# Kernel tuning notes

Measured on AMD Instinct MI355X. Metric: run time of the kernel, lower is better.

The kernel has to match this reference:

```python
import jax, jax.numpy as jnp
import numpy as np

H = 16      # q heads
G = 4       # groups (n_rep)
THETA = 10000.0


def _rope(x, cos, sin):
    # x pairs adjacent elements (torch complex view of reshape(..., -1, 2))
    x0 = x[..., ::2]
    x1 = x[..., 1::2]
    r0 = x0 * cos - x1 * sin
    r1 = x0 * sin + x1 * cos
    return jnp.stack([r0, r1], axis=-1).reshape(x.shape)


def setup_inputs() -> dict:
    key = jax.random.key(0)
    ks = jax.random.split(key, 5)
    B, S, D = 2, 2048, 1024
    return {
        "x": jax.random.normal(ks[0], (B, S, D), jnp.float32),
        "Wq": jax.random.normal(ks[1], (D, D), jnp.float32) * 0.02,
        "Wk": jax.random.normal(ks[2], (D, D // G), jnp.float32) * 0.02,
        "Wv": jax.random.normal(ks[3], (D, D // G), jnp.float32) * 0.02,
        "Wo": jax.random.normal(ks[4], (D, D), jnp.float32) * 0.02,
    }


def reference(x, Wq, Wk, Wv, Wo):
    B, S, D = x.shape
    hd = D // H                     # head dim = 64
    Hkv = H // G                    # kv heads = 4

    q = x @ Wq                      # (B,S,D)
    k = x @ Wk                      # (B,S,D/G)
    v = x @ Wv                      # (B,S,D/G)

    # repeat_kv: (B,S,Hkv,hd) -> (B,S,H,hd)
    k = jnp.repeat(k.reshape(B, S, Hkv, hd), G, axis=2)
    v = jnp.repeat(v.reshape(B, S, Hkv, hd), G, axis=2)

    # RoPE angles: freqs precomputed over hidden_dim (as in source)
    inv = 1.0 / (THETA ** (jnp.arange(0, D, 2, dtype=jnp.float32) / D))  # (D/2,)
    ang = jnp.arange(S, dtype=jnp.float32)[:, None] * inv[None, :]       # (S,D/2)
    q = _rope(q, jnp.cos(ang)[None], jnp.sin(ang)[None])                 # (B,S,D)
    angk = ang[:, : hd // 2]                                             # (S,hd/2)
    k = _rope(k, jnp.cos(angk)[None, :, None, :], jnp.sin(angk)[None, :, None, :])

    q = q.reshape(B, S, H, hd).transpose(0, 2, 1, 3)   # (B,H,S,hd)
    k = k.transpose(0, 2, 1, 3)
    v = v.transpose(0, 2, 1, 3)

    # NOTE: scale uses sqrt(hidden_dim), faithful to source
    scores = jnp.einsum('bhqd,bhkd->bhqk', q, k) / jnp.sqrt(jnp.float32(D))
    p = jax.nn.softmax(scores, axis=-1)
    o = jnp.einsum('bhqk,bhkd->bhqd', p, v)
    o = o.transpose(0, 2, 1, 3).reshape(B, S, D)
    return o @ Wo
```

## Files before the change

### kernel.cpp

```cpp
#include <hip/hip_runtime.h>
#include <math.h>

#define BATCH 2
#define SEQ   2048
#define DMODEL 1024
#define KDIM  1024
#define NH    16
#define HDIM  64
#define GRP   4
#define NKV   4

enum { M_PLAIN = 0, M_QKV = 1 };

#define LN_THETA 9.210340371976184f
#define QSCALE 0.04508422002778f

typedef short bf8_t __attribute__((ext_vector_type(8)));
typedef float f4_t __attribute__((ext_vector_type(4)));
typedef unsigned short us4_t __attribute__((ext_vector_type(4)));
typedef unsigned short us8_t __attribute__((ext_vector_type(8)));

#define QB_OFF 0
#define KB_OFF 4194304
#define VB_OFF (4194304 + 1048576)

__device__ __forceinline__ unsigned short f2bf(float f) {
  unsigned int u = __float_as_uint(f);
  u += 0x7fffu + ((u >> 16) & 1u);
  return (unsigned short)(u >> 16);
}

__device__ __forceinline__ float fexp2(float x) {
#if __has_builtin(__builtin_amdgcn_exp2f)
  return __builtin_amdgcn_exp2f(x);
#else
  return exp2f(x);
#endif
}

__device__ __forceinline__ void gload_lds16(const void* g, void* l) {
  typedef __attribute__((address_space(1))) unsigned int gu32;
  typedef __attribute__((address_space(3))) unsigned int lu32;
  __builtin_amdgcn_global_load_lds((const gu32*)g, (lu32*)l, 16, 0, 0);
}

__global__ __launch_bounds__(256) void convT_all(const float* __restrict__ W0,
                                                 const float* __restrict__ W1,
                                                 const float* __restrict__ W2,
                                                 const float* __restrict__ W3,
                                                 unsigned short* __restrict__ Wqkvt,
                                                 unsigned short* __restrict__ Wot) {
  const float* W; unsigned short* out; int N, rowoff;
  switch (blockIdx.z) {
    case 0: W = W0; out = Wqkvt; N = 1024; rowoff = 0;    break;
    case 1: W = W1; out = Wqkvt; N = 256;  rowoff = 1024; break;
    case 2: W = W2; out = Wqkvt; N = 256;  rowoff = 1280; break;
    default: W = W3; out = Wot;  N = 1024; rowoff = 0;    break;
  }
  const int n0 = blockIdx.x * 64;
  if (n0 >= N) return;
  __shared__ unsigned short T[64][72];
  const int t = threadIdx.x;
  const int k0 = blockIdx.y * 64;
  const int kr = t >> 4, n4 = (t & 15) * 4;
#pragma unroll
  for (int i = 0; i < 4; ++i) {
    const int k = kr + i * 16;
    float4 v = *(const float4*)&W[(size_t)(k0 + k) * N + n0 + n4];
    T[n4 + 0][k] = f2bf(v.x);
    T[n4 + 1][k] = f2bf(v.y);
    T[n4 + 2][k] = f2bf(v.z);
    T[n4 + 3][k] = f2bf(v.w);
  }
  __syncthreads();
#pragma unroll
  for (int i = 0; i < 2; ++i) {
    const int c = t + i * 256;
    const int n = c >> 3, kc = (c & 7) * 8;
    us8_t v = *(const us8_t*)&T[n][kc];
    *(us8_t*)&out[(size_t)(rowoff + n0 + n) * KDIM + k0 + kc] = v;
  }
}

template <int MODE>
__global__ __launch_bounds__(512, 2) void gemm_bf16(const void* __restrict__ A_,
                                                    const unsigned short* __restrict__ Bt,
                                                    void* __restrict__ Cdst_, int N) {
  __shared__ __align__(16) unsigned short As[4 * 4096];
  __shared__ __align__(16) unsigned short Bs[4 * 4096];

  const int tid = threadIdx.x;
  const int lane = tid & 63, quad = lane >> 4, l16 = lane & 15;
  const int w = tid >> 6, wm = w >> 1, wn = w & 1;
  const int row0 = blockIdx.x * 128, col0 = blockIdx.y * 128;

  const int m0 = tid >> 2;
  const int kc0 = (tid & 3) ^ ((m0 >> 1) & 3);
  const unsigned short* Ag0 = (const unsigned short*)A_ + (size_t)(row0 + m0) * KDIM + kc0 * 8;
  const float*          Xg0 = (const float*)A_ + (size_t)(row0 + m0) * KDIM + kc0 * 8;
  const unsigned short* Bg0 = Bt + (size_t)(col0 + m0) * KDIM + kc0 * 8;
  unsigned short* Al0 = &As[tid * 8];
  unsigned short* Bl0 = &Bs[tid * 8];

#define STAGE_GEMM(kk)                                                   \
  do {                                                                   \
    _Pragma("unroll") for (int kh = 0; kh < 4; ++kh) {                   \
      if constexpr (MODE == M_QKV) {                                     \
        float4 a0 = *(const float4*)(Xg0 + (kk) + kh * 32);              \
        float4 a1 = *(const float4*)(Xg0 + (kk) + kh * 32 + 4);          \
        us8_t o8 = {f2bf(a0.x), f2bf(a0.y), f2bf(a0.z), f2bf(a0.w),      \
                    f2bf(a1.x), f2bf(a1.y), f2bf(a1.z), f2bf(a1.w)};     \
        *(us8_t*)(Al0 + kh * 4096) = o8;                                 \
      } else {                                                           \
        gload_lds16(Ag0 + (kk) + kh * 32, Al0 + kh * 4096);              \
      }                                                                  \
      gload_lds16(Bg0 + (kk) + kh * 32, Bl0 + kh * 4096);                \
    }                                                                    \
  } while (0)

  int aoff[2][4], boff[4][4];
#pragma unroll
  for (int mi = 0; mi < 2; ++mi) {
    const int am = wm * 32 + mi * 16 + l16;
    const int sw = quad ^ ((am >> 1) & 3);
#pragma unroll
    for (int kh = 0; kh < 4; ++kh)
      aoff[mi][kh] = kh * 4096 + (((am << 2) | sw) << 3);
  }
#pragma unroll
  for (int ni = 0; ni < 4; ++ni) {
    const int bn = wn * 64 + ni * 16 + l16;
    const int sw = quad ^ ((bn >> 1) & 3);
#pragma unroll
    for (int kh = 0; kh < 4; ++kh)
      boff[ni][kh] = kh * 4096 + (((bn << 2) | sw) << 3);
  }

  f4_t acc[2][4];
#pragma unroll
  for (int mi = 0; mi < 2; ++mi)
#pragma unroll
    for (int ni = 0; ni < 4; ++ni) acc[mi][ni] = (f4_t){0.f, 0.f, 0.f, 0.f};

  for (int kb = 0; kb < KDIM; kb += 128) {
    __syncthreads();
    STAGE_GEMM(kb);
    __syncthreads();

#pragma unroll
    for (int kh = 0; kh < 4; ++kh) {
      bf8_t af[2], bfr[4];
#pragma unroll
      for (int mi = 0; mi < 2; ++mi) af[mi] = *(const bf8_t*)&As[aoff[mi][kh]];
#pragma unroll
      for (int ni = 0; ni < 4; ++ni) bfr[ni] = *(const bf8_t*)&Bs[boff[ni][kh]];
#pragma unroll
      for (int mi = 0; mi < 2; ++mi)
#pragma unroll
        for (int ni = 0; ni < 4; ++ni)
          acc[mi][ni] = __builtin_amdgcn_mfma_f32_16x16x32_bf16(af[mi], bfr[ni], acc[mi][ni], 0, 0, 0);
    }
  }
#undef STAGE_GEMM

  if constexpr (MODE == M_PLAIN) {
    float* out = (float*)Cdst_;
#pragma unroll
    for (int mi = 0; mi < 2; ++mi) {
      const int rowb = row0 + wm * 32 + mi * 16 + quad * 4;
#pragma unroll
      for (int ni = 0; ni < 4; ++ni) {
        const int n = col0 + wn * 64 + ni * 16 + l16;
#pragma unroll
        for (int r = 0; r < 4; ++r)
          out[(size_t)(rowb + r) * N + n] = acc[mi][ni][r];
      }
    }
  } else {
    unsigned short* Qb = (unsigned short*)Cdst_;
    unsigned short* Kb = Qb + (KB_OFF - QB_OFF);
    unsigned short* Vb = Qb + (VB_OFF - QB_OFF);
#pragma unroll
    for (int ni = 0; ni < 4; ++ni) {
      const int nb = col0 + wn * 64 + ni * 16;
      const int n = nb + l16;
      if (nb < 1024) {
        const float inv = expf(-(float)(2 * (n >> 1)) * (LN_THETA / (float)DMODEL));
        const float sgn = (n & 1) ? 1.f : -1.f;
        const int h = n >> 6, d = n & 63;
#pragma unroll
        for (int mi = 0; mi < 2; ++mi) {
          const int rowb = row0 + wm * 32 + mi * 16 + quad * 4;
#pragma unroll
          for (int r = 0; r < 4; ++r) {
            const int row = rowb + r;
            const int bb = row >> 11, s = row & (SEQ - 1);
            const float v = acc[mi][ni][r];
            const float p = __shfl_xor(v, 1);
            float sn, cs;
            sincosf((float)s * inv, &sn, &cs);
            const float res = (v * cs + sgn * p * sn) * QSCALE;
            Qb[((size_t)(bb * NH + h) * SEQ + s) * HDIM + d] = f2bf(res);
          }
        }
      } else if (nb < 1280) {
        const int nk = n - 1024;
        const int hkv = nk >> 6, d = nk & 63;
        const float inv = expf(-(float)(2 * (d >> 1)) * (LN_THETA / (float)DMODEL));
        const float sgn = (nk & 1) ? 1.f : -1.f;
#pragma unroll
        for (int mi = 0; mi < 2; ++mi) {
          const int rowb = row0 + wm * 32 + mi * 16 + quad * 4;
#pragma unroll
          for (int r = 0; r < 4; ++r) {
            const int row = rowb + r;
            const int bb = row >> 11, s = row & (SEQ - 1);
            const float v = acc[mi][ni][r];
            const float p = __shfl_xor(v, 1);
            float sn, cs;
            sincosf((float)s * inv, &sn, &cs);
            const float res = v * cs + sgn * p * sn;
            Kb[((size_t)(bb * NKV + hkv) * SEQ + s) * HDIM + d] = f2bf(res);
          }
        }
      } else {
        const int nv = n - 1280;
        const int hkv = nv >> 6, d = nv & 63;
#pragma unroll
        for (int mi = 0; mi < 2; ++mi) {
          const int s0 = row0 + wm * 32 + mi * 16 + quad * 4;
          const int bb = s0 >> 11, sl = s0 & (SEQ - 1);
          const int st = sl & 63;
          const int ps = (sl & ~63) | (st & 0x20) | ((st & 0x0C) << 1) | ((st & 0x10) >> 2);
          us4_t stv = {f2bf(acc[mi][ni][0]), f2bf(acc[mi][ni][1]),
                       f2bf(acc[mi][ni][2]), f2bf(acc[mi][ni][3])};
          *(us4_t*)&Vb[((size_t)(bb * NKV + hkv) * HDIM + d) * SEQ + ps] = stv;
        }
      }
    }
  }
}

__global__ __launch_bounds__(256, 4) void attn_fwd(const unsigned short* __restrict__ Q,
                                                   const unsigned short* __restrict__ K,
                                                   const unsigned short* __restrict__ V,
                                                   unsigned short* __restrict__ Ow) {
  __shared__ __align__(16) unsigned short Kt[2 * 4096];
  __shared__ __align__(16) unsigned short Vt[2 * 4096];

  const int b = blockIdx.x >> 4;
  const int h = blockIdx.x & (NH - 1);
  const int hkv = h >> 2;
  const int q0 = blockIdx.y * 128;
  const int tid = threadIdx.x;
  const int w = tid >> 6;
  const int lane = tid & 63;
  const int quad = lane >> 4;
  const int l16 = lane & 15;

  const unsigned short* Qg = Q + ((size_t)(b * NH + h) * SEQ + q0 + w * 32) * HDIM;
  const unsigned short* Kg = K + (size_t)(b * NKV + hkv) * SEQ * HDIM;
  const unsigned short* Vg = V + (size_t)(b * NKV + hkv) * HDIM * SEQ;

  bf8_t qb[2][2];
#pragma unroll
  for (int g = 0; g < 2; ++g)
#pragma unroll
    for (int half = 0; half < 2; ++half)
      qb[g][half] = *(const bf8_t*)(Qg + (size_t)(g * 16 + l16) * HDIM + half * 32 + quad * 8);

  f4_t accO[2][4];
#pragma unroll
  for (int g = 0; g < 2; ++g)
#pragma unroll
    for (int d = 0; d < 4; ++d) accO[g][d] = (f4_t){0.f, 0.f, 0.f, 0.f};
  float accLs[2] = {0.f, 0.f};

  const int sw8 = (quad ^ ((l16 >> 1) & 3)) << 3;

  const int skey = tid >> 2;
  const int gc = ((tid & 3) ^ ((tid >> 3) & 3)) << 3;
  const unsigned short* KgA = Kg + (size_t)skey * HDIM + gc;
  const unsigned short* VgA = Vg + (size_t)skey * SEQ + gc;

#define STAGE_ATTN(c, kk)                                                          \
  do {                                                                             \
    gload_lds16(KgA + (size_t)(kk) * HDIM,      &Kt[(c) * 4096 + tid * 8]);        \
    gload_lds16(KgA + (size_t)(kk) * HDIM + 32, &Kt[(c) * 4096 + tid * 8 + 2048]); \
    gload_lds16(VgA + (kk),      &Vt[(c) * 4096 + tid * 8]);                       \
    gload_lds16(VgA + (kk) + 32, &Vt[(c) * 4096 + tid * 8 + 2048]);                \
  } while (0)

  STAGE_ATTN(0, 0);
  __syncthreads();
  int cur = 0;
  for (int k0 = 0; k0 < SEQ; k0 += 64) {
    if (k0 + 64 < SEQ) STAGE_ATTN(cur ^ 1, k0 + 64);

    const unsigned short* Ktc = Kt + cur * 4096;
    const unsigned short* Vtc = Vt + cur * 4096;

    union { bf8_t bf; unsigned int dw[4]; } pa[2][2];
#pragma unroll
    for (int cb = 0; cb < 4; ++cb) {
      const int koff = (cb * 16 + l16) * 32 + sw8;
      bf8_t kf0 = *(const bf8_t*)&Ktc[koff];
      bf8_t kf1 = *(const bf8_t*)&Ktc[koff + 2048];
#pragma unroll
      for (int g = 0; g < 2; ++g) {
        f4_t s = (f4_t){0.f, 0.f, 0.f, 0.f};
        s = __builtin_amdgcn_mfma_f32_16x16x32_bf16(kf0, qb[g][0], s, 0, 0, 0);
        s = __builtin_amdgcn_mfma_f32_16x16x32_bf16(kf1, qb[g][1], s, 0, 0, 0);
        const float p0 = fexp2(s[0]), p1 = fexp2(s[1]);
        const float p2 = fexp2(s[2]), p3 = fexp2(s[3]);
        accLs[g] += (p0 + p1) + (p2 + p3);
        unsigned int w0, w1;
        asm("v_cvt_pk_bf16_f32 %0, %1, %2" : "=v"(w0) : "v"(p0), "v"(p1));
        asm("v_cvt_pk_bf16_f32 %0, %1, %2" : "=v"(w1) : "v"(p2), "v"(p3));
        pa[g][cb >> 1].dw[(cb & 1) * 2 + 0] = w0;
        pa[g][cb >> 1].dw[(cb & 1) * 2 + 1] = w1;
      }
    }

#pragma unroll
    for (int db = 0; db < 4; ++db) {
      const int voff = (db * 16 + l16) * 32 + sw8;
      bf8_t vf0 = *(const bf8_t*)&Vtc[voff];
      bf8_t vf1 = *(const bf8_t*)&Vtc[voff + 2048];
#pragma unroll
      for (int g = 0; g < 2; ++g) {
        accO[g][db] = __builtin_amdgcn_mfma_f32_16x16x32_bf16(pa[g][0].bf, vf0, accO[g][db], 0, 0, 0);
        accO[g][db] = __builtin_amdgcn_mfma_f32_16x16x32_bf16(pa[g][1].bf, vf1, accO[g][db], 0, 0, 0);
      }
    }

    __syncthreads();
    cur ^= 1;
  }
#undef STAGE_ATTN

#pragma unroll
  for (int g = 0; g < 2; ++g) {
    accLs[g] += __shfl_xor(accLs[g], 16);
    accLs[g] += __shfl_xor(accLs[g], 32);
  }
  const float il0 = 1.0f / accLs[0];
  const float il1 = 1.0f / accLs[1];

#pragma unroll
  for (int g = 0; g < 2; ++g)
#pragma unroll
    for (int r = 0; r < 4; ++r) {
      const float ilr = __shfl(g ? il1 : il0, quad * 4 + r);
      const int q = q0 + w * 32 + g * 16 + quad * 4 + r;
      unsigned short* op = Ow + (((size_t)b * SEQ + q) * NH + h) * HDIM;
#pragma unroll
      for (int db = 0; db < 4; ++db)
        op[db * 16 + l16] = f2bf(accO[g][db][r] * ilr);
    }
}

extern "C" void kernel_launch(void* const* d_in, const int* in_sizes, int n_in,
                              void* d_out, int out_size, void* d_ws, size_t ws_size,
                              hipStream_t stream) {
  (void)in_sizes; (void)n_in; (void)out_size; (void)ws_size;
  const float* x  = (const float*)d_in[0];
  const float* Wq = (const float*)d_in[1];
  const float* Wk = (const float*)d_in[2];
  const float* Wv = (const float*)d_in[3];
  const float* Wo = (const float*)d_in[4];
  float* out = (float*)d_out;

  unsigned short* Qb    = (unsigned short*)d_ws;
  unsigned short* Kb    = Qb + 4194304;
  unsigned short* Vb    = Kb + 1048576;
  unsigned short* Owb   = Vb + 1048576;
  unsigned short* Wqkvt = Owb + 4194304;
  unsigned short* Wot   = Wqkvt + 1572864;

  dim3 blk(256);
  convT_all<<<dim3(16, 16, 4), blk, 0, stream>>>(Wq, Wk, Wv, Wo, Wqkvt, Wot);

  gemm_bf16<M_QKV><<<dim3(32, 12), dim3(512), 0, stream>>>(x, Wqkvt, Qb, 1536);
  attn_fwd<<<dim3(BATCH * NH, SEQ / 128), blk, 0, stream>>>(Qb, Kb, Vb, Owb);
  gemm_bf16<M_PLAIN><<<dim3(32, 8), dim3(512), 0, stream>>>(Owb, Wot, out, DMODEL);
}
```

Baseline: 163.8 us.

## Double-buffer GEMM LDS staging, pre-convert x to bf16, prioritize attention MFMAs

```diff
diff --git a/kernel.cpp b/kernel.cpp
--- a/kernel.cpp
+++ b/kernel.cpp
@@ -42,6 +42,14 @@
   typedef __attribute__((address_space(1))) unsigned int gu32;
   typedef __attribute__((address_space(3))) unsigned int lu32;
   __builtin_amdgcn_global_load_lds((const gu32*)g, (lu32*)l, 16, 0, 0);
+}
+
+__global__ __launch_bounds__(256) void conv_x(const float* __restrict__ in,
+                                              unsigned short* __restrict__ out) {
+  const int i = blockIdx.x * 256 + threadIdx.x;
+  float4 v = ((const float4*)in)[i];
+  us4_t o = {f2bf(v.x), f2bf(v.y), f2bf(v.z), f2bf(v.w)};
+  ((us4_t*)out)[i] = o;
 }
 
 __global__ __launch_bounds__(256) void convT_all(const float* __restrict__ W0,
@@ -83,11 +91,11 @@
 }
 
 template <int MODE>
-__global__ __launch_bounds__(512, 2) void gemm_bf16(const void* __restrict__ A_,
+__global__ __launch_bounds__(512, 2) void gemm_bf16(const unsigned short* __restrict__ A,
                                                     const unsigned short* __restrict__ Bt,
                                                     void* __restrict__ Cdst_, int N) {
-  __shared__ __align__(16) unsigned short As[4 * 4096];
-  __shared__ __align__(16) unsigned short Bs[4 * 4096];
+  __shared__ __align__(16) unsigned short As[2 * 8192];
+  __shared__ __align__(16) unsigned short Bs[2 * 8192];
 
   const int tid = threadIdx.x;
   const int lane = tid & 63, quad = lane >> 4, l16 = lane & 15;
@@ -96,35 +104,26 @@
 
   const int m0 = tid >> 2;
   const int kc0 = (tid & 3) ^ ((m0 >> 1) & 3);
-  const unsigned short* Ag0 = (const unsigned short*)A_ + (size_t)(row0 + m0) * KDIM + kc0 * 8;
-  const float*          Xg0 = (const float*)A_ + (size_t)(row0 + m0) * KDIM + kc0 * 8;
+  const unsigned short* Ag0 = A + (size_t)(row0 + m0) * KDIM + kc0 * 8;
   const unsigned short* Bg0 = Bt + (size_t)(col0 + m0) * KDIM + kc0 * 8;
   unsigned short* Al0 = &As[tid * 8];
   unsigned short* Bl0 = &Bs[tid * 8];
 
-#define STAGE_GEMM(kk)                                                   \
-  do {                                                                   \
-    _Pragma("unroll") for (int kh = 0; kh < 4; ++kh) {                   \
-      if constexpr (MODE == M_QKV) {                                     \
-        float4 a0 = *(const float4*)(Xg0 + (kk) + kh * 32);              \
-        float4 a1 = *(const float4*)(Xg0 + (kk) + kh * 32 + 4);          \
-        us8_t o8 = {f2bf(a0.x), f2bf(a0.y), f2bf(a0.z), f2bf(a0.w),      \
-                    f2bf(a1.x), f2bf(a1.y), f2bf(a1.z), f2bf(a1.w)};     \
-        *(us8_t*)(Al0 + kh * 4096) = o8;                                 \
-      } else {                                                           \
-        gload_lds16(Ag0 + (kk) + kh * 32, Al0 + kh * 4096);              \
-      }                                                                  \
-      gload_lds16(Bg0 + (kk) + kh * 32, Bl0 + kh * 4096);                \
-    }                                                                    \
+#define STAGE_GEMM(c, kk)                                        \
+  do {                                                           \
+    gload_lds16(Ag0 + (kk),      Al0 + (c) * 8192);              \
+    gload_lds16(Ag0 + (kk) + 32, Al0 + (c) * 8192 + 4096);       \
+    gload_lds16(Bg0 + (kk),      Bl0 + (c) * 8192);              \
+    gload_lds16(Bg0 + (kk) + 32, Bl0 + (c) * 8192 + 4096);       \
   } while (0)
 
-  int aoff[2][4], boff[4][4];
+  int aoff[2][2], boff[4][2];
 #pragma unroll
   for (int mi = 0; mi < 2; ++mi) {
     const int am = wm * 32 + mi * 16 + l16;
     const int sw = quad ^ ((am >> 1) & 3);
 #pragma unroll
-    for (int kh = 0; kh < 4; ++kh)
+    for (int kh = 0; kh < 2; ++kh)
       aoff[mi][kh] = kh * 4096 + (((am << 2) | sw) << 3);
   }
 #pragma unroll
@@ -132,7 +131,7 @@
     const int bn = wn * 64 + ni * 16 + l16;
     const int sw = quad ^ ((bn >> 1) & 3);
 #pragma unroll
-    for (int kh = 0; kh < 4; ++kh)
+    for (int kh = 0; kh < 2; ++kh)
       boff[ni][kh] = kh * 4096 + (((bn << 2) | sw) << 3);
   }
 
@@ -142,24 +141,36 @@
 #pragma unroll
     for (int ni = 0; ni < 4; ++ni) acc[mi][ni] = (f4_t){0.f, 0.f, 0.f, 0.f};
 
-  for (int kb = 0; kb < KDIM; kb += 128) {
-    __syncthreads();
-    STAGE_GEMM(kb);
-    __syncthreads();
-
-#pragma unroll
-    for (int kh = 0; kh < 4; ++kh) {
+  STAGE_GEMM(0, 0);
+  int cur = 0;
+  for (int kb = 0; kb < KDIM; kb += 64) {
+    if (kb + 64 < KDIM) {
+      STAGE_GEMM(cur ^ 1, kb + 64);
+      asm volatile("s_waitcnt vmcnt(4)" ::: "memory");
+    } else {
+      asm volatile("s_waitcnt vmcnt(0)" ::: "memory");
+    }
+    __builtin_amdgcn_sched_barrier(0);
+    __builtin_amdgcn_s_barrier();
+
+    const unsigned short* Asc = As + cur * 8192;
+    const unsigned short* Bsc = Bs + cur * 8192;
+#pragma unroll
+    for (int kh = 0; kh < 2; ++kh) {
       bf8_t af[2], bfr[4];
 #pragma unroll
-      for (int mi = 0; mi < 2; ++mi) af[mi] = *(const bf8_t*)&As[aoff[mi][kh]];
-#pragma unroll
-      for (int ni = 0; ni < 4; ++ni) bfr[ni] = *(const bf8_t*)&Bs[boff[ni][kh]];
+      for (int mi = 0; mi < 2; ++mi) af[mi] = *(const bf8_t*)&Asc[aoff[mi][kh]];
+#pragma unroll
+      for (int ni = 0; ni < 4; ++ni) bfr[ni] = *(const bf8_t*)&Bsc[boff[ni][kh]];
 #pragma unroll
       for (int mi = 0; mi < 2; ++mi)
 #pragma unroll
         for (int ni = 0; ni < 4; ++ni)
           acc[mi][ni] = __builtin_amdgcn_mfma_f32_16x16x32_bf16(af[mi], bfr[ni], acc[mi][ni], 0, 0, 0);
     }
+    __builtin_amdgcn_sched_barrier(0);
+    __builtin_amdgcn_s_barrier();
+    cur ^= 1;
   }
 #undef STAGE_GEMM
 
@@ -309,8 +320,10 @@
 #pragma unroll
       for (int g = 0; g < 2; ++g) {
         f4_t s = (f4_t){0.f, 0.f, 0.f, 0.f};
+        __builtin_amdgcn_s_setprio(1);
         s = __builtin_amdgcn_mfma_f32_16x16x32_bf16(kf0, qb[g][0], s, 0, 0, 0);
         s = __builtin_amdgcn_mfma_f32_16x16x32_bf16(kf1, qb[g][1], s, 0, 0, 0);
+        __builtin_amdgcn_s_setprio(0);
         const float p0 = fexp2(s[0]), p1 = fexp2(s[1]);
         const float p2 = fexp2(s[2]), p3 = fexp2(s[3]);
         accLs[g] += (p0 + p1) + (p2 + p3);
@@ -322,6 +335,7 @@
       }
     }
 
+    __builtin_amdgcn_s_setprio(1);
 #pragma unroll
     for (int db = 0; db < 4; ++db) {
       const int voff = (db * 16 + l16) * 32 + sw8;
@@ -333,6 +347,7 @@
         accO[g][db] = __builtin_amdgcn_mfma_f32_16x16x32_bf16(pa[g][1].bf, vf1, accO[g][db], 0, 0, 0);
       }
     }
+    __builtin_amdgcn_s_setprio(0);
 
     __syncthreads();
     cur ^= 1;
@@ -375,13 +390,15 @@
   unsigned short* Kb    = Qb + 4194304;
   unsigned short* Vb    = Kb + 1048576;
   unsigned short* Owb   = Vb + 1048576;
-  unsigned short* Wqkvt = Owb + 4194304;
+  unsigned short* xb    = Owb + 4194304;
+  unsigned short* Wqkvt = xb + 4194304;
   unsigned short* Wot   = Wqkvt + 1572864;
 
   dim3 blk(256);
+  conv_x<<<dim3(4096), blk, 0, stream>>>(x, xb);
   convT_all<<<dim3(16, 16, 4), blk, 0, stream>>>(Wq, Wk, Wv, Wo, Wqkvt, Wot);
 
-  gemm_bf16<M_QKV><<<dim3(32, 12), dim3(512), 0, stream>>>(x, Wqkvt, Qb, 1536);
+  gemm_bf16<M_QKV><<<dim3(32, 12), dim3(512), 0, stream>>>(xb, Wqkvt, Qb, 1536);
   attn_fwd<<<dim3(BATCH * NH, SEQ / 128), blk, 0, stream>>>(Qb, Kb, Vb, Owb);
   gemm_bf16<M_PLAIN><<<dim3(32, 8), dim3(512), 0, stream>>>(Owb, Wot, out, DMODEL);
 }
```

Result: no change. 164.0 us (+0.1%).
